# Kernel tuning notes

Hardware: AMD Instinct MI355X
Metric: run time of the kernel (lower is better)

## Reference

```python
import jax, jax.numpy as jnp
from jax import lax
import numpy as np

D_MODEL = 1024; N_HEADS = 16; D_K = 64; D_FF = 4096
D_STATE = 16; D_CONV = 4; D_INNER = 2048; EPS = 1e-5
BATCH = 2; SEQ = 2048


def _ln(x, g, b):
    m = x.mean(-1, keepdims=True)
    v = ((x - m) ** 2).mean(-1, keepdims=True)
    return (x - m) * lax.rsqrt(v + EPS) * g + b


def setup_inputs() -> dict:
    key = jax.random.key(0)
    ks = jax.random.split(key, 12)
    rn = lambda k, sh, s=0.02: jax.random.normal(k, sh, jnp.float32) * s
    return {
        'x': jax.random.normal(ks[0], (BATCH, SEQ, D_MODEL), jnp.float32),
        'ln1_g': jnp.ones(D_MODEL), 'ln1_b': jnp.zeros(D_MODEL),
        'Wq': rn(ks[1], (D_MODEL, D_MODEL)), 'bq': jnp.zeros(D_MODEL),
        'Wk': rn(ks[2], (D_MODEL, D_MODEL)), 'bk': jnp.zeros(D_MODEL),
        'Wv': rn(ks[3], (D_MODEL, D_MODEL)), 'bv': jnp.zeros(D_MODEL),
        'Wo': rn(ks[4], (D_MODEL, D_MODEL)), 'bo': jnp.zeros(D_MODEL),
        'ln2_g': jnp.ones(D_MODEL), 'ln2_b': jnp.zeros(D_MODEL),
        'in_w': rn(ks[5], (D_MODEL, 2 * D_INNER)), 'in_b': jnp.zeros(2 * D_INNER),
        'conv_w': rn(ks[6], (D_INNER, 1, D_CONV), 0.2), 'conv_b': jnp.zeros(D_INNER),
        'xp_w': rn(ks[7], (D_INNER, 2 * D_STATE)), 'xp_b': jnp.zeros(2 * D_STATE),
        'dt': rn(ks[8], (D_INNER,), 0.1), 'A': rn(ks[9], (D_STATE, D_STATE), 0.1),
        'Dp': jnp.ones(D_INNER),
        'out_w': rn(ks[10], (D_INNER, D_MODEL)), 'out_b': jnp.zeros(D_MODEL),
        'ln3_g': jnp.ones(D_MODEL), 'ln3_b': jnp.zeros(D_MODEL),
        'fc1_w': rn(ks[11], (D_MODEL, D_FF)), 'fc1_b': jnp.zeros(D_FF),
        'fc2_w': rn(jax.random.fold_in(key, 99), (D_FF, D_MODEL)), 'fc2_b': jnp.zeros(D_MODEL),
    }


def reference(x, ln1_g, ln1_b, Wq, bq, Wk, bk, Wv, bv, Wo, bo, ln2_g, ln2_b,
              in_w, in_b, conv_w, conv_b, xp_w, xp_b, dt, A, Dp, out_w, out_b,
              ln3_g, ln3_b, fc1_w, fc1_b, fc2_w, fc2_b):
    Bsz, S, _ = x.shape
    # --- attention (block sliding-window mask == full causal mask) ---
    h = _ln(x, ln1_g, ln1_b)
    q = (h @ Wq + bq).reshape(Bsz, S, N_HEADS, D_K).transpose(0, 2, 1, 3)
    k = (h @ Wk + bk).reshape(Bsz, S, N_HEADS, D_K).transpose(0, 2, 1, 3)
    v = (h @ Wv + bv).reshape(Bsz, S, N_HEADS, D_K).transpose(0, 2, 1, 3)
    scores = jnp.einsum('bhqd,bhkd->bhqk', q, k) / float(D_K ** 0.5)
    causal = jnp.tril(jnp.ones((S, S), bool))
    scores = jnp.where(causal, scores, -jnp.inf)
    probs = jax.nn.softmax(scores, axis=-1)
    attn = jnp.einsum('bhqk,bhkd->bhqd', probs, v).transpose(0, 2, 1, 3).reshape(Bsz, S, D_MODEL)
    x = x + attn @ Wo + bo
    # --- Mamba-style layer ---
    h = _ln(x, ln2_g, ln2_b)
    xr = h @ in_w + in_b                      # (B,S,2*Di)
    xm, res = xr[..., :D_INNER], xr[..., D_INNER:]
    # causal depthwise conv: torch Conv1d(pad=d_conv-1)[..., :S] == left-pad conv
    xc = lax.conv_general_dilated(xm.transpose(0, 2, 1), conv_w, (1,), [(D_CONV - 1, 0)],
                                  dimension_numbers=('NCH', 'OIH', 'NCH'),
                                  feature_group_count=D_INNER)
    xm = jax.nn.silu((xc + conv_b[None, :, None]).transpose(0, 2, 1))
    xdbl = xm @ xp_w + xp_b                   # (B,S,2*d_state)
    Bm, Cm = xdbl[..., :D_STATE], xdbl[..., D_STATE:]
    # dt = exp(param)[:d_state], indexed by i % d_state per step (as in source)
    dts = jnp.exp(dt)[:D_STATE][jnp.arange(S) % D_STATE]  # (S,)
    # NOTE: the source scan never uses u = x[:,i,:] (and hence D); hs depends
    # only on dt, A, B, C — replicated faithfully here.

    def step(hst, inp):
        d_t, b_t, c_t = inp
        A_t = jnp.exp(d_t * A)                # (d_state,d_state)
        hst = jnp.tanh(hst @ A_t.T) + b_t * hst + c_t
        return hst, hst

    h0 = jnp.zeros((Bsz, D_STATE), x.dtype)
    _, hs = lax.scan(step, h0, (dts, Bm.transpose(1, 0, 2), Cm.transpose(1, 0, 2)))
    hs = hs.transpose(1, 0, 2)                # (B,S,d_state)
    y = jnp.repeat(hs, D_INNER // D_STATE, axis=-1) + res
    x = x + y @ out_w + out_b
    # --- FFN (tanh-approx GELU) ---
    h = _ln(x, ln3_g, ln3_b)
    x = x + jax.nn.gelu(h @ fc1_w + fc1_b, approximate=True) @ fc2_w + fc2_b
    return x
```

## Files before the change

kernel.cpp:

```cpp
#include <hip/hip_runtime.h>
#include <hip/hip_bf16.h>


#define SEQ     2048
#define BATCH   2
#define MROWS   4096
#define DMODEL  1024
#define DINNER  2048
#define DFF     4096
#define QKVLD   3072

typedef __attribute__((ext_vector_type(8))) short bf16x8;
typedef __attribute__((ext_vector_type(4))) float f32x4;
typedef __attribute__((ext_vector_type(2))) __fp16 f16x2;

__device__ __forceinline__ unsigned short f2b(float x){
    __hip_bfloat16 h = __float2bfloat16(x);
    return *reinterpret_cast<unsigned short*>(&h);
}
__device__ __forceinline__ float b2f(unsigned short u){
    __hip_bfloat16 h;
    *reinterpret_cast<unsigned short*>(&h) = u;
    return __bfloat162float(h);
}
__device__ __forceinline__ float gelu_f(float v){
    float u = 0.7978845608f*(v + 0.044715f*v*v*v);
    float e = __expf(2.f*u);
    float th = 1.f - 2.f*__builtin_amdgcn_rcpf(e + 1.f);
    return 0.5f*v*(1.f + th);
}
__device__ __forceinline__ void gload16(const unsigned short* g, unsigned short* l){
    __builtin_amdgcn_global_load_lds(
        (const __attribute__((address_space(1))) void*)g,
        (__attribute__((address_space(3))) void*)l, 16, 0, 0);
}
template<int CTRL>
__device__ __forceinline__ float dppf(float x){
    int r = __builtin_amdgcn_mov_dpp(__builtin_bit_cast(int, x), CTRL, 0xf, 0xf, false);
    return __builtin_bit_cast(float, r);
}
template<int CTRL>
__device__ __forceinline__ int dppi(int x){
    return __builtin_amdgcn_mov_dpp(x, CTRL, 0xf, 0xf, false);
}
template<int CTRL>
__device__ __forceinline__ f16x2 dpp_h2(f16x2 x){
    int r = __builtin_amdgcn_mov_dpp(__builtin_bit_cast(int, x), CTRL, 0xf, 0xf, false);
    return __builtin_bit_cast(f16x2, r);
}

#if __has_builtin(__builtin_amdgcn_exp2f)
#define W_SCALE 2.8853900817779268f
__device__ __forceinline__ float exp_2s(float x){ return __builtin_amdgcn_exp2f(x); }
#else
#define W_SCALE 2.0f
__device__ __forceinline__ float exp_2s(float x){ return __expf(x); }
#endif

__device__ __forceinline__ float hdot2(f16x2 a, f16x2 b, float c){
#if __has_builtin(__builtin_amdgcn_fdot2)
    return __builtin_amdgcn_fdot2(a, b, c, false);
#else
    return c + (float)a[0]*(float)b[0] + (float)a[1]*(float)b[1];
#endif
}
__device__ __forceinline__ f16x2 u2h(unsigned u){ return __builtin_bit_cast(f16x2, u); }

__device__ __forceinline__ void tc_body(
    const float* __restrict__ W, unsigned short* __restrict__ Wt, int K, int N)
{
    __shared__ float t[64*65];
    int n0 = blockIdx.x*64, k0 = blockIdx.y*64;
    int c = threadIdx.x & 63, r0 = threadIdx.x >> 6;
    #pragma unroll
    for (int rr = 0; rr < 64; rr += 4)
        t[(rr+r0)*65 + c] = W[(size_t)(k0+rr+r0)*N + n0 + c];
    __syncthreads();
    #pragma unroll
    for (int rr = 0; rr < 64; rr += 4)
        Wt[(size_t)(n0+rr+r0)*K + k0 + c] = f2b(t[c*65 + rr + r0]);
}

__global__ __launch_bounds__(256) void transpose_cast(
    const float* __restrict__ W, unsigned short* __restrict__ Wt, int K, int N)
{
    tc_body(W, Wt, K, N);
}

__global__ __launch_bounds__(256) void transpose_cast4(
    const float* __restrict__ W0, const float* __restrict__ W1,
    const float* __restrict__ W2, const float* __restrict__ W3,
    unsigned short* __restrict__ T0, unsigned short* __restrict__ T1,
    unsigned short* __restrict__ T2, unsigned short* __restrict__ T3,
    int K, int N)
{
    const float* W; unsigned short* Wt;
    switch (blockIdx.z){
        case 0:  W = W0; Wt = T0; break;
        case 1:  W = W1; Wt = T1; break;
        case 2:  W = W2; Wt = T2; break;
        default: W = W3; Wt = T3; break;
    }
    tc_body(W, Wt, K, N);
}

__global__ __launch_bounds__(256) void transpose_cast2(
    const float* __restrict__ W0, const float* __restrict__ W1,
    unsigned short* __restrict__ T0, unsigned short* __restrict__ T1,
    int K, int N)
{
    const float* W = blockIdx.z ? W1 : W0;
    unsigned short* Wt = blockIdx.z ? T1 : T0;
    tc_body(W, Wt, K, N);
}

__global__ __launch_bounds__(256) void concat_bias(
    const float* __restrict__ b0, const float* __restrict__ b1,
    const float* __restrict__ b2, float* __restrict__ o)
{
    int t = blockIdx.x*256 + threadIdx.x;
    float v = (t < 1024) ? b0[t] : (t < 2048 ? b1[t-1024] : b2[t-2048]);
    o[t] = v;
}

__global__ __launch_bounds__(256) void layernorm_bf16(
    const float* __restrict__ x, const float* __restrict__ g,
    const float* __restrict__ b, unsigned short* __restrict__ out)
{
    int row = blockIdx.x;
    const float4* xr = (const float4*)(x + (size_t)row*DMODEL);
    int tid = threadIdx.x;
    float4 xv = xr[tid];
    float s  = xv.x + xv.y + xv.z + xv.w;
    float ss = xv.x*xv.x + xv.y*xv.y + xv.z*xv.z + xv.w*xv.w;
    #pragma unroll
    for (int d = 32; d > 0; d >>= 1){ s += __shfl_xor(s,d); ss += __shfl_xor(ss,d); }
    __shared__ float sm[8];
    int wv = tid>>6, ln = tid&63;
    if (ln == 0){ sm[wv] = s; sm[4+wv] = ss; }
    __syncthreads();
    s  = sm[0]+sm[1]+sm[2]+sm[3];
    ss = sm[4]+sm[5]+sm[6]+sm[7];
    float mean = s*(1.f/DMODEL);
    float var  = ss*(1.f/DMODEL) - mean*mean;
    float rstd = rsqrtf(var + 1e-5f);
    float4 gv = ((const float4*)g)[tid];
    float4 bv = ((const float4*)b)[tid];
    ushort4 o;
    o.x = f2b((xv.x-mean)*rstd*gv.x + bv.x);
    o.y = f2b((xv.y-mean)*rstd*gv.y + bv.y);
    o.z = f2b((xv.z-mean)*rstd*gv.z + bv.z);
    o.w = f2b((xv.w-mean)*rstd*gv.w + bv.w);
    ((ushort4*)(out + (size_t)row*DMODEL))[tid] = o;
}

template<int BN, int OUT_BF16, int HAS_RES, int ACT>
__global__ __launch_bounds__(256,3) void gemm_bt(
    const unsigned short* __restrict__ A, const unsigned short* __restrict__ Bt,
    const float* __restrict__ bias, const float* __restrict__ res,
    void* __restrict__ outp, int Ndim, int Kdim)
{
    constexpr int NT = BN/32;
    constexpr int BROWS = BN/32;
    __shared__ unsigned short As[128*64];
    __shared__ unsigned short Bs[BN*64];
    int tid = threadIdx.x;
    int lane = tid & 63, wv = tid >> 6;
    int l15 = lane & 15, quad = lane >> 4;
    int m0 = blockIdx.y*128, n0 = blockIdx.x*BN;
    int mo = (wv>>1)*64, no = (wv&1)*(BN/2);
    int rsub = (lane >> 3);
    int cc8  = (lane & 7)*8;
    f32x4 zz = {0.f,0.f,0.f,0.f};
    f32x4 acc[4][NT];
    #pragma unroll
    for (int i=0;i<4;++i)
      #pragma unroll
      for (int j=0;j<NT;++j) acc[i][j] = zz;

    for (int k0 = 0; k0 < Kdim; k0 += 64){
        const unsigned short* Ab = A  + (size_t)(m0 + wv*32 + rsub)*Kdim + k0 + cc8;
        const unsigned short* Bb = Bt + (size_t)(n0 + wv*(BN/4) + rsub)*Kdim + k0 + cc8;
        #pragma unroll
        for (int i=0;i<4;++i)
            gload16(Ab + (size_t)(i*8)*Kdim, &As[(wv*32 + i*8)*64]);
        #pragma unroll
        for (int i=0;i<BROWS;++i)
            gload16(Bb + (size_t)(i*8)*Kdim, &Bs[(wv*(BN/4) + i*8)*64]);
        __syncthreads();
        #pragma unroll
        for (int kc=0;kc<2;++kc){
            bf16x8 af[4], bfr[NT];
            #pragma unroll
            for (int t=0;t<4;++t)
                af[t]  = *(const bf16x8*)(&As[(mo + t*16 + l15)*64 + kc*32 + quad*8]);
            #pragma unroll
            for (int t=0;t<NT;++t)
                bfr[t] = *(const bf16x8*)(&Bs[(no + t*16 + l15)*64 + kc*32 + quad*8]);
            #pragma unroll
            for (int mt=0;mt<4;++mt)
              #pragma unroll
              for (int nt=0;nt<NT;++nt)
                acc[mt][nt] = __builtin_amdgcn_mfma_f32_16x16x32_bf16(af[mt], bfr[nt], acc[mt][nt], 0,0,0);
        }
        __syncthreads();
    }
    #pragma unroll
    for (int mt=0;mt<4;++mt){
      #pragma unroll
      for (int nt=0;nt<NT;++nt){
        int gn = n0 + no + nt*16 + l15;
        float bval = bias[gn];
        #pragma unroll
        for (int r=0;r<4;++r){
            int gm = m0 + mo + mt*16 + quad*4 + r;
            size_t off = (size_t)gm*Ndim + gn;
            float v = acc[mt][nt][r] + bval;
            if constexpr (HAS_RES) v += res[off];
            if constexpr (ACT == 1) v = gelu_f(v);
            if constexpr (OUT_BF16) ((unsigned short*)outp)[off] = f2b(v);
            else                    ((float*)outp)[off] = v;
        }
      }
    }
}

__global__ __launch_bounds__(256) void transpose_v(
    const unsigned short* __restrict__ qkv, unsigned short* __restrict__ vT)
{
    __shared__ unsigned int t[64*33];
    int bh = blockIdx.y;
    int t0 = blockIdx.x*64;
    int tid = threadIdx.x;
    const size_t base = (size_t)(bh>>4)*SEQ*QKVLD + (size_t)(bh&15)*64 + 2*DMODEL;
    #pragma unroll
    for (int i=0;i<2;++i){
        int idx = tid + i*256;
        int r = idx>>3, cc = idx&7;
        uint4 vv = *(const uint4*)(qkv + base + (size_t)(t0+r)*QKVLD + cc*8);
        t[r*33 + cc*4 + 0] = vv.x;
        t[r*33 + cc*4 + 1] = vv.y;
        t[r*33 + cc*4 + 2] = vv.z;
        t[r*33 + cc*4 + 3] = vv.w;
    }
    __syncthreads();
    unsigned short* outb = vT + (size_t)bh*64*SEQ + t0;
    #pragma unroll
    for (int i=0;i<2;++i){
        int idx = tid + i*256;
        int d = idx>>3, cc = idx&7;
        int sh = (d&1)*16, dp = d>>1;
        unsigned int o4[4];
        #pragma unroll
        for (int j2=0;j2<4;++j2){
            unsigned int ua = t[(cc*8 + 2*j2    )*33 + dp];
            unsigned int ub = t[(cc*8 + 2*j2 + 1)*33 + dp];
            unsigned int ha = (ua >> sh) & 0xffff;
            unsigned int hb = (ub >> sh) & 0xffff;
            o4[j2] = ha | (hb << 16);
        }
        *(uint4*)(outb + (size_t)d*SEQ + cc*8) = *(uint4*)o4;
    }
}

__device__ __forceinline__ void stage_kv(
    const unsigned short* __restrict__ k, const unsigned short* __restrict__ vTb,
    int t0, unsigned short* Ks, unsigned short* Vt, int wv, int lane)
{
    #pragma unroll
    for (int p=0;p<4;++p){
        int c0 = p*256 + wv*64;
        int c  = c0 + lane;
        int kr = c>>3, kc = (c&7)*8;
        int vr = c>>4, vc = (c&15)*8;
        gload16(k   + (size_t)(t0+kr)*QKVLD + (kc ^ ((kr&7)<<3)), Ks + c0*8);
        gload16(vTb + (size_t)vr*SEQ + t0 +   (vc ^ ((vr&7)<<3)), Vt + c0*8);
    }
}

__global__ __launch_bounds__(256,2) void attn_flash(
    const unsigned short* __restrict__ qkv, const unsigned short* __restrict__ vT,
    unsigned short* __restrict__ attn)
{
    __shared__ unsigned short Ks[2][128*64];
    __shared__ unsigned short Vt[2][64*128];
    __shared__ unsigned short Ps[64*128];
    int bh = blockIdx.y;
    int qt = (int)gridDim.x - 1 - (int)blockIdx.x;
    int q0 = qt*128;
    int tid = threadIdx.x, wv = tid>>6, lane = tid&63;
    int l15 = lane&15, quad = lane>>4;
    int xsw = (l15&7)<<3;
    const size_t basei = (size_t)(bh>>4)*SEQ*QKVLD + (size_t)(bh&15)*64;
    const unsigned short* q = qkv + basei;
    const unsigned short* k = qkv + basei + DMODEL;
    const unsigned short* vTb = vT + (size_t)bh*64*SEQ;
    const size_t baseo = (size_t)(bh>>4)*SEQ*DMODEL + (size_t)(bh&15)*64;

    int nkt = qt + 1;

    stage_kv(k, vTb, 0, Ks[0], Vt[0], wv, lane);

    bf16x8 aq[2][2];
    #pragma unroll
    for (int s=0;s<2;++s){
        int qr = q0 + wv*32 + s*16 + l15;
        aq[s][0] = *(const bf16x8*)(q + (size_t)qr*QKVLD + quad*8);
        aq[s][1] = *(const bf16x8*)(q + (size_t)qr*QKVLD + 32 + quad*8);
    }

    float m_i[2][4], l_i[2][4];
    f32x4 zz = {0.f,0.f,0.f,0.f};
    f32x4 o[2][4];
    #pragma unroll
    for (int s=0;s<2;++s)
      #pragma unroll
      for (int r=0;r<4;++r){ m_i[s][r] = -__builtin_inff(); l_i[s][r] = 0.f; }
    #pragma unroll
    for (int s=0;s<2;++s)
      #pragma unroll
      for (int d=0;d<4;++d) o[s][d] = zz;

    const float SCL = 0.1803368801111137f;

    asm volatile("s_waitcnt vmcnt(0)" ::: "memory");
    __builtin_amdgcn_s_barrier();

    for (int kt = 0; kt < nkt; ++kt){
        int t0 = kt*128;
        bool diagt = (kt == qt);
        int cur = kt & 1;
        const unsigned short* Kc = Ks[cur];
        const unsigned short* Vc = Vt[cur];

        if (kt + 1 < nkt){
            stage_kv(k, vTb, t0 + 128, Ks[cur^1], Vt[cur^1], wv, lane);
            asm volatile("s_waitcnt vmcnt(8)" ::: "memory");
        } else {
            asm volatile("s_waitcnt vmcnt(0)" ::: "memory");
        }
        __builtin_amdgcn_sched_barrier(0);
        __builtin_amdgcn_s_barrier();

        #pragma unroll
        for (int sub=0; sub<2; ++sub){
            f32x4 sc[8];
            #pragma unroll
            for (int st=0;st<8;++st){
                bf16x8 b0 = *(const bf16x8*)(&Kc[(st*16+l15)*64 + ((     quad*8) ^ xsw)]);
                bf16x8 b1 = *(const bf16x8*)(&Kc[(st*16+l15)*64 + ((32 + quad*8) ^ xsw)]);
                sc[st] = __builtin_amdgcn_mfma_f32_16x16x32_bf16(aq[sub][0], b0, zz, 0,0,0);
                sc[st] = __builtin_amdgcn_mfma_f32_16x16x32_bf16(aq[sub][1], b1, sc[st], 0,0,0);
            }
            int qrb = q0 + wv*32 + sub*16 + quad*4;
            float mrow[4];
            #pragma unroll
            for (int r=0;r<4;++r) mrow[r] = -__builtin_inff();
            #pragma unroll
            for (int st=0;st<8;++st)
              #pragma unroll
              for (int r=0;r<4;++r){
                float svv = sc[st][r]*SCL;
                if (diagt && (t0 + st*16 + l15 > qrb + r))
                    svv = -__builtin_inff();
                sc[st][r] = svv;
                mrow[r] = fmaxf(mrow[r], svv);
              }
            #pragma unroll
            for (int d=1; d<16; d<<=1)
              #pragma unroll
              for (int r=0;r<4;++r) mrow[r] = fmaxf(mrow[r], __shfl_xor(mrow[r], d));
            float alpha[4], rsum[4];
            #pragma unroll
            for (int r=0;r<4;++r){
                float mn = fmaxf(m_i[sub][r], mrow[r]);
                alpha[r] = exp_2s(m_i[sub][r] - mn);
                m_i[sub][r] = mn;
            }
            #pragma unroll
            for (int st=0;st<8;++st)
              #pragma unroll
              for (int r=0;r<4;++r) sc[st][r] = exp_2s(sc[st][r] - m_i[sub][r]);
            #pragma unroll
            for (int r=0;r<4;++r){
                rsum[r] = ((sc[0][r]+sc[1][r])+(sc[2][r]+sc[3][r]))
                        + ((sc[4][r]+sc[5][r])+(sc[6][r]+sc[7][r]));
            }
            #pragma unroll
            for (int d=1; d<16; d<<=1)
              #pragma unroll
              for (int r=0;r<4;++r) rsum[r] += __shfl_xor(rsum[r], d);
            #pragma unroll
            for (int r=0;r<4;++r) l_i[sub][r] = l_i[sub][r]*alpha[r] + rsum[r];
            #pragma unroll
            for (int st=0;st<8;++st)
              #pragma unroll
              for (int r=0;r<4;++r){
                int prow = wv*16 + quad*4 + r;
                Ps[prow*128 + ((st*16 + l15) ^ (((quad*4+r)&7)<<3))] = f2b(sc[st][r]);
              }
            #pragma unroll
            for (int d=0;d<4;++d)
              #pragma unroll
              for (int r=0;r<4;++r) o[sub][d][r] = o[sub][d][r]*alpha[r];

            bf16x8 ap[4];
            #pragma unroll
            for (int kch=0;kch<4;++kch)
                ap[kch] = *(const bf16x8*)(&Ps[(wv*16 + l15)*128 + ((kch*32 + quad*8) ^ xsw)]);
            #pragma unroll
            for (int dtile=0;dtile<4;++dtile){
                #pragma unroll
                for (int kch=0;kch<4;++kch){
                    bf16x8 bv_ = *(const bf16x8*)(&Vc[(dtile*16+l15)*128 + ((kch*32 + quad*8) ^ xsw)]);
                    o[sub][dtile] = __builtin_amdgcn_mfma_f32_16x16x32_bf16(ap[kch], bv_, o[sub][dtile], 0,0,0);
                }
            }
        }

        __builtin_amdgcn_s_barrier();
    }
    #pragma unroll
    for (int sub=0; sub<2; ++sub)
      #pragma unroll
      for (int r=0;r<4;++r){
        float inv = 1.f/l_i[sub][r];
        int gm = q0 + wv*32 + sub*16 + quad*4 + r;
        #pragma unroll
        for (int dtile=0;dtile<4;++dtile)
            attn[baseo + (size_t)gm*DMODEL + dtile*16 + l15] = f2b(o[sub][dtile][r]*inv);
      }
}

__global__ __launch_bounds__(256) void conv_silu(
    const unsigned short* __restrict__ xr, const float* __restrict__ cw,
    const float* __restrict__ cb, unsigned short* __restrict__ xm2)
{
    int idx = blockIdx.x*256 + threadIdx.x;
    int r  = idx >> 10;
    int c2 = (idx & 1023)*2;
    int s  = r & (SEQ-1);
    float4 w0 = *(const float4*)(cw + c2*4);
    float4 w1 = *(const float4*)(cw + (c2+1)*4);
    float w0a[4] = {w0.x,w0.y,w0.z,w0.w};
    float w1a[4] = {w1.x,w1.y,w1.z,w1.w};
    float a0 = cb[c2], a1 = cb[c2+1];
    const unsigned short* xrow = xr + (size_t)r*DFF + c2;
    #pragma unroll
    for (int j=0;j<4;++j){
        int sp = s - 3 + j;
        if (sp >= 0){
            int off = (j-3)*DFF;
            unsigned int u = *(const unsigned int*)(xrow + off);
            a0 += w0a[j]*b2f(u & 0xffff);
            a1 += w1a[j]*b2f(u >> 16);
        }
    }
    float s0 = a0 * __builtin_amdgcn_rcpf(1.f + __expf(-a0));
    float s1 = a1 * __builtin_amdgcn_rcpf(1.f + __expf(-a1));
    unsigned int op = (unsigned int)f2b(s0) | ((unsigned int)f2b(s1) << 16);
    *(unsigned int*)(xm2 + (size_t)r*DINNER + c2) = op;
}

__global__ __launch_bounds__(256) void xp_gemm(
    const unsigned short* __restrict__ xm2, const float* __restrict__ w,
    const float* __restrict__ bias, float* __restrict__ xdbl)
{
    int tid = threadIdx.x;
    int lr = tid >> 5, n = tid & 31;
    int row = blockIdx.x*8 + lr;
    const unsigned short* ar = xm2 + (size_t)row*DINNER;
    float acc = bias[n];
    #pragma unroll 4
    for (int k2 = 0; k2 < DINNER; k2 += 2){
        unsigned int u = *(const unsigned int*)(ar + k2);
        acc += b2f(u & 0xffff)*w[k2*32 + n] + b2f(u >> 16)*w[(k2+1)*32 + n];
    }
    if (n >= 16) acc += 1.f;
    int nc = (n < 16) ? 2*n : 2*(n-16)+1;
    xdbl[(size_t)row*32 + nc] = acc;
}

__device__ __forceinline__ float scan_step_lds(float h, const float* lwp,
                                               float bv, float cv)
{
    uint4 wa = *(const uint4*)(lwp);
    uint4 wb = *(const uint4*)(lwp + 4);
    float rr = dppf<0x121>(h);
    f16x2 p0 = __builtin_amdgcn_cvt_pkrtz(h, rr);
    f16x2 p1 = dpp_h2<0x122>(p0);
    f16x2 p2 = dpp_h2<0x124>(p0);
    f16x2 p3 = dpp_h2<0x126>(p0);
    f16x2 p4 = dpp_h2<0x128>(p0);
    f16x2 p5 = dpp_h2<0x12a>(p0);
    f16x2 p6 = dpp_h2<0x12c>(p0);
    f16x2 p7 = dpp_h2<0x12e>(p0);
    float a0 = hdot2(u2h(wa.x), p0, 0.f);
    a0 = hdot2(u2h(wa.y), p1, a0);
    a0 = hdot2(u2h(wa.z), p2, a0);
    a0 = hdot2(u2h(wa.w), p3, a0);
    float a1 = hdot2(u2h(wb.x), p4, 0.f);
    a1 = hdot2(u2h(wb.y), p5, a1);
    a1 = hdot2(u2h(wb.z), p6, a1);
    a1 = hdot2(u2h(wb.w), p7, a1);
    float u  = fmaf(bv, h, cv);
    float e2 = exp_2s(a0 + a1);
    float r  = __builtin_amdgcn_rcpf(e2 + 1.f);
    return fmaf(-2.f, r, u);
}

__device__ __forceinline__ void load_bank(float2 (&bk)[16], const float* src){
    #pragma unroll
    for (int j=0;j<16;++j) bk[j] = *(const float2*)(src + (size_t)j*32);
}

__device__ __forceinline__ void compute16(const float2 (&bk)[16],
                                          const float* __restrict__ lw_i,
                                          float& hn, float* hp, int lane)
{
    float h0s=0.f, h1s=0.f, h2s=0.f;
    #pragma unroll
    for (int j=0;j<16;++j){
        hn = scan_step_lds(hn, lw_i + j*192, bk[j].x, bk[j].y);
        if ((j&3)==0)      h0s = hn;
        else if ((j&3)==1) h1s = hn;
        else if ((j&3)==2) h2s = hn;
        else if (lane < 16){
            float4 o4 = {h0s, h1s, h2s, hn};
            *(float4*)(hp + j - 3) = o4;
        }
    }
}

__global__ __launch_bounds__(128,1) void scan_k(
    const float* __restrict__ xdbl, const float* __restrict__ dt,
    const float* __restrict__ A, float* __restrict__ hsT)
{
    __shared__ float lw[16*192];
    int tid = threadIdx.x;
    int lane = tid & 63;
    int b = tid >> 6;
    int i = lane & 15;

    int c1 = dppi<0x121>(i);
    int sj[8], tj[8];
    sj[0] = i;               tj[0] = c1;
    sj[1] = dppi<0x122>(i);  tj[1] = dppi<0x122>(c1);
    sj[2] = dppi<0x124>(i);  tj[2] = dppi<0x124>(c1);
    sj[3] = dppi<0x126>(i);  tj[3] = dppi<0x126>(c1);
    sj[4] = dppi<0x128>(i);  tj[4] = dppi<0x128>(c1);
    sj[5] = dppi<0x12a>(i);  tj[5] = dppi<0x12a>(c1);
    sj[6] = dppi<0x12c>(i);  tj[6] = dppi<0x12c>(c1);
    sj[7] = dppi<0x12e>(i);  tj[7] = dppi<0x12e>(c1);

    int grp = tid >> 4;
    #pragma unroll
    for (int pp=0; pp<2; ++pp){
        int p = grp*2 + pp;
        float dtp = __expf(dt[p]);
        #pragma unroll
        for (int jj=0;jj<8;++jj){
            float w0 = W_SCALE*__expf(dtp * A[i*16 + sj[jj]]);
            float w1 = W_SCALE*__expf(dtp * A[i*16 + tj[jj]]);
            f16x2 pk = __builtin_amdgcn_cvt_pkrtz(w0, w1);
            lw[p*192 + i*12 + jj] = __builtin_bit_cast(float, pk);
        }
    }
    __syncthreads();

    const float* src = xdbl + (size_t)(b*SEQ)*32 + 2*i;
    const float* lw_i = lw + i*12;
    float* hp = hsT + (size_t)(b*16 + i)*SEQ;
    float2 bA[16], bB[16];
    load_bank(bA, src);
    float hn = 0.f;
    for (int bp = 0; bp < 64; ++bp){
        int t0 = bp*32;
        load_bank(bB, src + (size_t)(t0+16)*32);
        compute16(bA, lw_i, hn, hp + t0, lane);
        int t2 = (bp < 63) ? (t0 + 32) : 0;
        load_bank(bA, src + (size_t)t2*32);
        compute16(bB, lw_i, hn, hp + t0 + 16, lane);
    }
}

__global__ __launch_bounds__(256) void y_assemble(
    const float* __restrict__ hsT, const unsigned short* __restrict__ xr,
    unsigned short* __restrict__ y)
{
    int idx = blockIdx.x*256 + threadIdx.x;
    int r = idx >> 10;
    int c2 = (idx & 1023)*2;
    int bb = r >> 11, s = r & (SEQ-1);
    unsigned int u = *(const unsigned int*)(xr + (size_t)r*DFF + DINNER + c2);
    float h0 = hsT[(size_t)(bb*16 + (c2 >> 7))*SEQ + s];
    float y0 = h0 + b2f(u & 0xffff);
    float y1 = h0 + b2f(u >> 16);
    *(unsigned int*)(y + (size_t)r*DINNER + c2) =
        (unsigned int)f2b(y0) | ((unsigned int)f2b(y1) << 16);
}

extern "C" void kernel_launch(void* const* d_in, const int* in_sizes, int n_in,
                              void* d_out, int out_size, void* d_ws, size_t ws_size,
                              hipStream_t stream)
{
    (void)in_sizes; (void)n_in; (void)out_size; (void)ws_size;
    const float* x     = (const float*)d_in[0];
    const float* ln1_g = (const float*)d_in[1];
    const float* ln1_b = (const float*)d_in[2];
    const float* Wq    = (const float*)d_in[3];
    const float* bq    = (const float*)d_in[4];
    const float* Wk    = (const float*)d_in[5];
    const float* bk    = (const float*)d_in[6];
    const float* Wv    = (const float*)d_in[7];
    const float* bv    = (const float*)d_in[8];
    const float* Wo    = (const float*)d_in[9];
    const float* bo    = (const float*)d_in[10];
    const float* ln2_g = (const float*)d_in[11];
    const float* ln2_b = (const float*)d_in[12];
    const float* in_w  = (const float*)d_in[13];
    const float* in_b  = (const float*)d_in[14];
    const float* conv_w= (const float*)d_in[15];
    const float* conv_b= (const float*)d_in[16];
    const float* xp_w  = (const float*)d_in[17];
    const float* xp_b  = (const float*)d_in[18];
    const float* dt    = (const float*)d_in[19];
    const float* A     = (const float*)d_in[20];
    const float* out_w = (const float*)d_in[22];
    const float* out_b = (const float*)d_in[23];
    const float* ln3_g = (const float*)d_in[24];
    const float* ln3_b = (const float*)d_in[25];
    const float* fc1_w = (const float*)d_in[26];
    const float* fc1_b = (const float*)d_in[27];
    const float* fc2_w = (const float*)d_in[28];
    const float* fc2_b = (const float*)d_in[29];

    char* ws = (char*)d_ws;
    const size_t MB = 1ull << 20;
    unsigned short* qkvT = (unsigned short*)(ws + 0*MB);
    unsigned short* WoT  = (unsigned short*)(ws + 6*MB);
    unsigned short* inT  = (unsigned short*)(ws + 8*MB);
    unsigned short* outT = (unsigned short*)(ws + 16*MB);
    unsigned short* f1T  = (unsigned short*)(ws + 20*MB);
    unsigned short* f2T  = (unsigned short*)(ws + 28*MB);
    unsigned short* hbf  = (unsigned short*)(ws + 36*MB);
    float*          x2   = (float*)(ws + 44*MB);
    float*          x3   = (float*)(ws + 60*MB);
    unsigned short* qkv  = (unsigned short*)(ws + 76*MB);
    unsigned short* attnb= (unsigned short*)(ws + 100*MB);
    unsigned short* xr   = (unsigned short*)(ws + 76*MB);
    unsigned short* ffn  = (unsigned short*)(ws + 76*MB);
    unsigned short* xm2  = (unsigned short*)(ws + 108*MB);
    unsigned short* yb   = (unsigned short*)(ws + 108*MB);
    float*          xdbl = (float*)(ws + 124*MB);
    float*          hsb  = (float*)(ws + 124*MB + 512*1024);
    float*          bqkv = (float*)(ws + 125*MB);

    dim3 blk(256);
    transpose_cast4<<<dim3(16,16,4), blk, 0, stream>>>(
        Wq, Wk, Wv, Wo,
        qkvT, qkvT + 1024*1024, qkvT + 2*1024*1024, WoT, 1024, 1024);
    transpose_cast2<<<dim3(64,16,2), blk, 0, stream>>>(in_w, fc1_w, inT, f1T, 1024, 4096);
    transpose_cast<<<dim3(16,32), blk, 0, stream>>>(out_w, outT, 2048, 1024);
    transpose_cast<<<dim3(16,64), blk, 0, stream>>>(fc2_w, f2T, 4096, 1024);
    concat_bias<<<12, blk, 0, stream>>>(bq, bk, bv, bqkv);

    layernorm_bf16<<<MROWS, blk, 0, stream>>>(x, ln1_g, ln1_b, hbf);
    gemm_bt<128,1,0,0><<<dim3(24,32), blk, 0, stream>>>(hbf, qkvT, bqkv, nullptr, qkv, QKVLD, 1024);
    transpose_v<<<dim3(32,32), blk, 0, stream>>>(qkv, hbf);
    attn_flash<<<dim3(16,32), blk, 0, stream>>>(qkv, hbf, attnb);
    gemm_bt<64,0,1,0><<<dim3(16,32), blk, 0, stream>>>(attnb, WoT, bo, x, x2, 1024, 1024);
    layernorm_bf16<<<MROWS, blk, 0, stream>>>(x2, ln2_g, ln2_b, hbf);
    gemm_bt<128,1,0,0><<<dim3(32,32), blk, 0, stream>>>(hbf, inT, in_b, nullptr, xr, 4096, 1024);
    conv_silu<<<16384, blk, 0, stream>>>(xr, conv_w, conv_b, xm2);
    xp_gemm<<<512, blk, 0, stream>>>(xm2, xp_w, xp_b, xdbl);
    scan_k<<<1, dim3(128), 0, stream>>>(xdbl, dt, A, hsb);
    y_assemble<<<16384, blk, 0, stream>>>(hsb, xr, yb);
    gemm_bt<64,0,1,0><<<dim3(16,32), blk, 0, stream>>>(yb, outT, out_b, x2, x3, 1024, 2048);
    layernorm_bf16<<<MROWS, blk, 0, stream>>>(x3, ln3_g, ln3_b, hbf);
    gemm_bt<128,1,0,1><<<dim3(32,32), blk, 0, stream>>>(hbf, f1T, fc1_b, nullptr, ffn, 4096, 1024);
    gemm_bt<64,0,1,0><<<dim3(16,32), blk, 0, stream>>>(ffn, f2T, fc2_b, x3, (float*)d_out, 1024, 4096);
}
```

Before: 850.1 us.

## Overlap serial scan with out-proj GEMM and apply hs via pooled weights

Splits y@out_w into res@out_w plus hs@pooled(out_w), where out_w is summed over each 128-row group that a repeated state channel maps to. The residual half of the GEMM now reads xr directly with a stride, which removes the y_assemble pass. That GEMM runs in the same launch as the single-block serial scan, so the scan is hidden behind GEMM blocks. A small hs_add kernel then applies the rank-16 hs correction in fp32. This adds a pooling kernel and an extra read-modify-write pass over x3, and it changes rounding because hs is no longer cast to bf16 before the GEMM.

```diff
diff --git a/kernel.cpp b/kernel.cpp
--- a/kernel.cpp
+++ b/kernel.cpp
@@ -112,6 +112,18 @@
     const float* W = blockIdx.z ? W1 : W0;
     unsigned short* Wt = blockIdx.z ? T1 : T0;
     tc_body(W, Wt, K, N);
+}
+
+__global__ __launch_bounds__(256) void pool_outw(
+    const float* __restrict__ W, float* __restrict__ Wp)
+{
+    int idx = blockIdx.x*256 + threadIdx.x;
+    int n = idx & 1023, i = idx >> 10;
+    const float* col = W + (size_t)(i*128)*DMODEL + n;
+    float s = 0.f;
+    #pragma unroll 8
+    for (int j=0;j<128;++j) s += col[(size_t)j*DMODEL];
+    Wp[i*DMODEL + n] = s;
 }
 
 __global__ __launch_bounds__(256) void concat_bias(
@@ -155,19 +167,17 @@
 }
 
 template<int BN, int OUT_BF16, int HAS_RES, int ACT>
-__global__ __launch_bounds__(256,3) void gemm_bt(
+__device__ __forceinline__ void gemm_core(
     const unsigned short* __restrict__ A, const unsigned short* __restrict__ Bt,
     const float* __restrict__ bias, const float* __restrict__ res,
-    void* __restrict__ outp, int Ndim, int Kdim)
+    void* __restrict__ outp, int Ndim, int Kdim, int Astr,
+    int m0, int n0, unsigned short* As, unsigned short* Bs)
 {
     constexpr int NT = BN/32;
     constexpr int BROWS = BN/32;
-    __shared__ unsigned short As[128*64];
-    __shared__ unsigned short Bs[BN*64];
     int tid = threadIdx.x;
     int lane = tid & 63, wv = tid >> 6;
     int l15 = lane & 15, quad = lane >> 4;
-    int m0 = blockIdx.y*128, n0 = blockIdx.x*BN;
     int mo = (wv>>1)*64, no = (wv&1)*(BN/2);
     int rsub = (lane >> 3);
     int cc8  = (lane & 7)*8;
@@ -179,11 +189,11 @@
       for (int j=0;j<NT;++j) acc[i][j] = zz;
 
     for (int k0 = 0; k0 < Kdim; k0 += 64){
-        const unsigned short* Ab = A  + (size_t)(m0 + wv*32 + rsub)*Kdim + k0 + cc8;
+        const unsigned short* Ab = A  + (size_t)(m0 + wv*32 + rsub)*Astr + k0 + cc8;
         const unsigned short* Bb = Bt + (size_t)(n0 + wv*(BN/4) + rsub)*Kdim + k0 + cc8;
         #pragma unroll
         for (int i=0;i<4;++i)
-            gload16(Ab + (size_t)(i*8)*Kdim, &As[(wv*32 + i*8)*64]);
+            gload16(Ab + (size_t)(i*8)*Astr, &As[(wv*32 + i*8)*64]);
         #pragma unroll
         for (int i=0;i<BROWS;++i)
             gload16(Bb + (size_t)(i*8)*Kdim, &Bs[(wv*(BN/4) + i*8)*64]);
@@ -223,6 +233,18 @@
         }
       }
     }
+}
+
+template<int BN, int OUT_BF16, int HAS_RES, int ACT>
+__global__ __launch_bounds__(256,3) void gemm_bt(
+    const unsigned short* __restrict__ A, const unsigned short* __restrict__ Bt,
+    const float* __restrict__ bias, const float* __restrict__ res,
+    void* __restrict__ outp, int Ndim, int Kdim)
+{
+    __shared__ unsigned short As[128*64];
+    __shared__ unsigned short Bs[BN*64];
+    gemm_core<BN,OUT_BF16,HAS_RES,ACT>(A, Bt, bias, res, outp, Ndim, Kdim, Kdim,
+                                       blockIdx.y*128, blockIdx.x*BN, As, Bs);
 }
 
 __global__ __launch_bounds__(256) void transpose_v(
@@ -532,11 +554,11 @@
     }
 }
 
-__global__ __launch_bounds__(128,1) void scan_k(
-    const float* __restrict__ xdbl, const float* __restrict__ dt,
-    const float* __restrict__ A, float* __restrict__ hsT)
-{
-    __shared__ float lw[16*192];
+__device__ void scan_body(const float* __restrict__ xdbl,
+                          const float* __restrict__ dt,
+                          const float* __restrict__ A,
+                          float* __restrict__ hsT, float* lw)
+{
     int tid = threadIdx.x;
     int lane = tid & 63;
     int b = tid >> 6;
@@ -553,10 +575,8 @@
     sj[6] = dppi<0x12c>(i);  tj[6] = dppi<0x12c>(c1);
     sj[7] = dppi<0x12e>(i);  tj[7] = dppi<0x12e>(c1);
 
-    int grp = tid >> 4;
-    #pragma unroll
-    for (int pp=0; pp<2; ++pp){
-        int p = grp*2 + pp;
+    {
+        int p = tid >> 4;
         float dtp = __expf(dt[p]);
         #pragma unroll
         for (int jj=0;jj<8;++jj){
@@ -567,6 +587,7 @@
         }
     }
     __syncthreads();
+    if (b >= 2) return;
 
     const float* src = xdbl + (size_t)(b*SEQ)*32 + 2*i;
     const float* lw_i = lw + i*12;
@@ -584,20 +605,39 @@
     }
 }
 
-__global__ __launch_bounds__(256) void y_assemble(
-    const float* __restrict__ hsT, const unsigned short* __restrict__ xr,
-    unsigned short* __restrict__ y)
+__global__ __launch_bounds__(256,3) void scan_out_gemm(
+    const float* __restrict__ xdbl, const float* __restrict__ dt,
+    const float* __restrict__ Amat, float* __restrict__ hsT,
+    const unsigned short* __restrict__ resA, const unsigned short* __restrict__ outT,
+    const float* __restrict__ out_b, const float* __restrict__ x2,
+    float* __restrict__ x3)
+{
+    __shared__ unsigned short As[128*64];
+    __shared__ unsigned short Bs[64*64];
+    __shared__ float lw[16*192];
+    if (blockIdx.x == 0){
+        scan_body(xdbl, dt, Amat, hsT, lw);
+    } else {
+        int bx = (int)blockIdx.x - 1;
+        gemm_core<64,0,1,0>(resA, outT, out_b, x2, x3, DMODEL, DINNER, DFF,
+                            (bx>>4)*128, (bx&15)*64, As, Bs);
+    }
+}
+
+__global__ __launch_bounds__(256) void hs_add(
+    const float* __restrict__ hsT, const float* __restrict__ Wp,
+    float* __restrict__ x3)
 {
     int idx = blockIdx.x*256 + threadIdx.x;
+    int c = idx & 1023;
     int r = idx >> 10;
-    int c2 = (idx & 1023)*2;
     int bb = r >> 11, s = r & (SEQ-1);
-    unsigned int u = *(const unsigned int*)(xr + (size_t)r*DFF + DINNER + c2);
-    float h0 = hsT[(size_t)(bb*16 + (c2 >> 7))*SEQ + s];
-    float y0 = h0 + b2f(u & 0xffff);
-    float y1 = h0 + b2f(u >> 16);
-    *(unsigned int*)(y + (size_t)r*DINNER + c2) =
-        (unsigned int)f2b(y0) | ((unsigned int)f2b(y1) << 16);
+    const float* hp = hsT + (size_t)bb*16*SEQ + s;
+    float acc = x3[(size_t)r*DMODEL + c];
+    #pragma unroll
+    for (int i=0;i<16;++i)
+        acc = fmaf(hp[(size_t)i*SEQ], Wp[i*DMODEL + c], acc);
+    x3[(size_t)r*DMODEL + c] = acc;
 }
 
 extern "C" void kernel_launch(void* const* d_in, const int* in_sizes, int n_in,
@@ -651,10 +691,10 @@
     unsigned short* xr   = (unsigned short*)(ws + 76*MB);
     unsigned short* ffn  = (unsigned short*)(ws + 76*MB);
     unsigned short* xm2  = (unsigned short*)(ws + 108*MB);
-    unsigned short* yb   = (unsigned short*)(ws + 108*MB);
     float*          xdbl = (float*)(ws + 124*MB);
     float*          hsb  = (float*)(ws + 124*MB + 512*1024);
     float*          bqkv = (float*)(ws + 125*MB);
+    float*          wpool= (float*)(ws + 126*MB);
 
     dim3 blk(256);
     transpose_cast4<<<dim3(16,16,4), blk, 0, stream>>>(
@@ -663,6 +703,7 @@
     transpose_cast2<<<dim3(64,16,2), blk, 0, stream>>>(in_w, fc1_w, inT, f1T, 1024, 4096);
     transpose_cast<<<dim3(16,32), blk, 0, stream>>>(out_w, outT, 2048, 1024);
     transpose_cast<<<dim3(16,64), blk, 0, stream>>>(fc2_w, f2T, 4096, 1024);
+    pool_outw<<<64, blk, 0, stream>>>(out_w, wpool);
     concat_bias<<<12, blk, 0, stream>>>(bq, bk, bv, bqkv);
 
     layernorm_bf16<<<MROWS, blk, 0, stream>>>(x, ln1_g, ln1_b, hbf);
@@ -674,9 +715,9 @@
     gemm_bt<128,1,0,0><<<dim3(32,32), blk, 0, stream>>>(hbf, inT, in_b, nullptr, xr, 4096, 1024);
     conv_silu<<<16384, blk, 0, stream>>>(xr, conv_w, conv_b, xm2);
     xp_gemm<<<512, blk, 0, stream>>>(xm2, xp_w, xp_b, xdbl);
-    scan_k<<<1, dim3(128), 0, stream>>>(xdbl, dt, A, hsb);
-    y_assemble<<<16384, blk, 0, stream>>>(hsb, xr, yb);
-    gemm_bt<64,0,1,0><<<dim3(16,32), blk, 0, stream>>>(yb, outT, out_b, x2, x3, 1024, 2048);
+    scan_out_gemm<<<513, blk, 0, stream>>>(xdbl, dt, A, hsb,
+                                           xr + DINNER, outT, out_b, x2, x3);
+    hs_add<<<16384, blk, 0, stream>>>(hsb, wpool, x3);
     layernorm_bf16<<<MROWS, blk, 0, stream>>>(x3, ln3_g, ln3_b, hbf);
     gemm_bt<128,1,0,1><<<dim3(32,32), blk, 0, stream>>>(hbf, f1T, fc1_b, nullptr, ffn, 4096, 1024);
     gemm_bt<64,0,1,0><<<dim3(16,32), blk, 0, stream>>>(ffn, f2T, fc2_b, x3, (float*)d_out, 1024, 4096);
```

Result: slower. 1.022 ms (+20.2%).
